# Kernel optimization log

Hardware: AMD Instinct MI355X
Metric: run time of the kernel (lower is better)

The kernel has to match this reference:

```python
import jax, jax.numpy as jnp
import numpy as np

TEMPERATURE = 0.07
CONCEPT_WEIGHT = 0.5
CONCEPT_SIM_WEIGHT = 0.3


def setup_inputs() -> dict:
    key = jax.random.key(0)
    k1, k2, k3, k4, k5 = jax.random.split(key, 5)
    B, C = 512, 256
    return {
        "logits_per_image": jax.random.normal(k1, (B, B), dtype=jnp.float32) * 3.0,
        "logits_per_text": jax.random.normal(k2, (B, B), dtype=jnp.float32) * 3.0,
        "concepts_logits": jax.random.normal(k3, (B, C), dtype=jnp.float32),
        "concepts_image_similarity": jax.random.normal(k4, (B, B), dtype=jnp.float32),
        # medical concepts in {-1 (missing), 0, 1}
        "medical_concepts": jax.random.randint(k5, (B, C), -1, 2, dtype=jnp.int32),
    }


def _clip_loss(logits_per_image, logits_per_text):
    # cross_entropy with labels = arange(B): -mean(diag(log_softmax))
    lp_img = jax.nn.log_softmax(logits_per_image, axis=1)
    lp_txt = jax.nn.log_softmax(logits_per_text, axis=1)
    image_loss = -jnp.mean(jnp.diagonal(lp_img))
    text_loss = -jnp.mean(jnp.diagonal(lp_txt))
    return (image_loss + text_loss) / 2.0


def _concept_classification_loss(concepts_logits, medical_concepts):
    mask = (medical_concepts != -1).astype(jnp.float32)
    targets = jnp.where(medical_concepts == -1, 0, medical_concepts).astype(jnp.float32)
    # BCEWithLogits (no pos_weight): logaddexp(0, x) - x*t  (numerically stable)
    loss = jnp.logaddexp(0.0, concepts_logits) - concepts_logits * targets
    return (loss * mask).sum() / (mask.sum() + 1e-8)


def _concept_similarity_loss(concepts_image_sim, medical_concepts):
    B = medical_concepts.shape[0]
    w = jnp.where(medical_concepts == -1, 0, medical_concepts).astype(jnp.float32)  # [B,C]
    # vectorized pairwise Jaccard (replaces O(B^2) python loop)
    intersection = jnp.minimum(w[:, None, :], w[None, :, :]).sum(-1)  # [B,B]
    union = jnp.maximum(w[:, None, :], w[None, :, :]).sum(-1)  # [B,B]
    sim = jnp.where(union > 0, intersection / jnp.where(union > 0, union, 1.0), 0.0)
    targets = jax.nn.softmax(sim / TEMPERATURE, axis=1)  # [B,B]
    log_probs = jax.nn.log_softmax(concepts_image_sim, axis=1)
    # kl_div(log_probs, targets, reduction='batchmean')
    kl = jnp.sum(targets * (jnp.log(targets) - log_probs)) / B
    return kl


def reference(logits_per_image, logits_per_text, concepts_logits,
              concepts_image_similarity, medical_concepts):
    clip_loss = _clip_loss(logits_per_image, logits_per_text)
    concept_loss = _concept_classification_loss(concepts_logits, medical_concepts)
    concept_sim_loss = _concept_similarity_loss(concepts_image_similarity, medical_concepts)
    total_loss = clip_loss + CONCEPT_WEIGHT * concept_loss + CONCEPT_SIM_WEIGHT * concept_sim_loss
    return total_loss
```

## Files before the change

kernel.cpp:

```cpp
#include <hip/hip_runtime.h>
#include <cstdint>

#define BSZ 512
#define CSZ 256


__device__ __forceinline__ float wave_sum64(float v) {
    #pragma unroll
    for (int o = 32; o > 0; o >>= 1) v += __shfl_xor(v, o, 64);
    return v;
}

__device__ __forceinline__ float block_sum(float v, float* s4) {
    v = wave_sum64(v);
    if ((threadIdx.x & 63) == 0) s4[threadIdx.x >> 6] = v;
    __syncthreads();
    float r = (s4[0] + s4[1]) + (s4[2] + s4[3]);
    __syncthreads();
    return r;
}

__global__ void __launch_bounds__(256)
prep(const float* __restrict__ img, const float* __restrict__ txt,
     const float* __restrict__ clog, const int* __restrict__ mc,
     char* __restrict__ ws) {
    __shared__ float s4[4];
    int g = blockIdx.x, tid = threadIdx.x;
    float* pc = (float*)(ws + 1024);
    float* pb = (float*)(ws + 5120);
    float* pm = (float*)(ws + 7168);
    unsigned long long* packed = (unsigned long long*)(ws + 12288);

    if (g == 0) ((unsigned int*)ws)[tid] = 0u;

    if (g < 1024) {
        int b = g & 511;
        const float* row = ((g < 512) ? img : txt) + (size_t)b * BSZ;
        float2 v = ((const float2*)row)[tid];
        float S = block_sum(expf(v.x) + expf(v.y), s4);
        if (tid == 0) pc[g] = logf(S) - row[b];
    } else {
        int b = g - 1024;
        int m = mc[b * CSZ + tid];
        float x = clog[b * CSZ + tid];
        float maskf = (m != -1) ? 1.0f : 0.0f;
        float t = (m == 1) ? 1.0f : 0.0f;
        float loss = (fmaxf(x, 0.0f) + log1pf(expf(-fabsf(x))) - x * t) * maskf;
        float Ls = block_sum(loss, s4);
        float Ms = block_sum(maskf, s4);
        if (tid == 0) { pb[b] = Ls; pm[b] = Ms; }
        unsigned long long bal = __ballot(m == 1);
        if ((tid & 63) == 0) packed[b * 4 + (tid >> 6)] = bal;
    }
}

__global__ void __launch_bounds__(256)
simfin(const float* __restrict__ csim, char* __restrict__ ws,
       float* __restrict__ out) {
    __shared__ float s4[4];
    __shared__ int islast;

    unsigned int* dc = (unsigned int*)ws;
    unsigned int* d2 = (unsigned int*)(ws + 512);
    float* pc = (float*)(ws + 1024);
    float* pb = (float*)(ws + 5120);
    float* pm = (float*)(ws + 7168);
    float* pk = (float*)(ws + 9216);
    const unsigned long long* packed = (const unsigned long long*)(ws + 12288);

    int b = blockIdx.x, tid = threadIdx.x;

    unsigned long long a0 = packed[b * 4 + 0], a1 = packed[b * 4 + 1];
    unsigned long long a2 = packed[b * 4 + 2], a3 = packed[b * 4 + 3];
    const ulonglong2* p2 = (const ulonglong2*)packed;
    ulonglong2 r0 = p2[4 * tid + 0], r1 = p2[4 * tid + 1];
    ulonglong2 r2 = p2[4 * tid + 2], r3 = p2[4 * tid + 3];
    float2 cv = ((const float2*)(csim + (size_t)b * BSZ))[tid];

    int i0 = __popcll(a0 & r0.x) + __popcll(a1 & r0.y) + __popcll(a2 & r1.x) + __popcll(a3 & r1.y);
    int u0 = __popcll(a0 | r0.x) + __popcll(a1 | r0.y) + __popcll(a2 | r1.x) + __popcll(a3 | r1.y);
    int i1 = __popcll(a0 & r2.x) + __popcll(a1 & r2.y) + __popcll(a2 & r3.x) + __popcll(a3 & r3.y);
    int u1 = __popcll(a0 | r2.x) + __popcll(a1 | r2.y) + __popcll(a2 | r3.x) + __popcll(a3 | r3.y);
    float s0 = ((u0 > 0) ? ((float)i0 / (float)u0) : 0.0f) * (1.0f / 0.07f);
    float s1 = ((u1 > 0) ? ((float)i1 / (float)u1) : 0.0f) * (1.0f / 0.07f);
    float c0 = cv.x, c1 = cv.y;

    float Zs = block_sum(expf(s0) + expf(s1), s4);
    float Zc = block_sum(expf(c0) + expf(c1), s4);
    float lse_s = logf(Zs), lse_c = logf(Zc);
    float t0 = expf(s0 - lse_s), t1 = expf(s1 - lse_s);
    float kl = block_sum(t0 * ((s0 - lse_s) - (c0 - lse_c)) +
                         t1 * ((s1 - lse_s) - (c1 - lse_c)), s4);

    if (tid == 0) {
        __hip_atomic_store(&pk[b], kl, __ATOMIC_RELAXED, __HIP_MEMORY_SCOPE_AGENT);
        __threadfence();
        islast = 0;
        unsigned t1k = atomicAdd(&dc[(b & 7) * 16], 1u);
        if (t1k == 63u) {
            unsigned t2k = atomicAdd(d2, 1u);
            if (t2k == 7u) islast = 1;
        }
    }
    __syncthreads();

    if (islast) {
        __threadfence();
        float sc = 0.0f, sb = 0.0f, sm = 0.0f, sk = 0.0f;
        for (int k = tid; k < 2 * BSZ; k += 256) sc += pc[k];
        for (int k = tid; k < BSZ; k += 256) {
            sb += pb[k];
            sm += pm[k];
            sk += __hip_atomic_load(&pk[k], __ATOMIC_RELAXED, __HIP_MEMORY_SCOPE_AGENT);
        }
        sc = block_sum(sc, s4);
        sb = block_sum(sb, s4);
        sm = block_sum(sm, s4);
        sk = block_sum(sk, s4);
        if (tid == 0) {
            out[0] = sc / (2.0f * BSZ)
                   + 0.5f * (sb / (sm + 1e-8f))
                   + 0.3f * (sk / (float)BSZ);
        }
    }
}

extern "C" void kernel_launch(void* const* d_in, const int* in_sizes, int n_in,
                              void* d_out, int out_size, void* d_ws, size_t ws_size,
                              hipStream_t stream) {
    const float* logits_img = (const float*)d_in[0];
    const float* logits_txt = (const float*)d_in[1];
    const float* clog       = (const float*)d_in[2];
    const float* csim       = (const float*)d_in[3];
    const int*   mc         = (const int*)d_in[4];
    float* out = (float*)d_out;
    char* ws = (char*)d_ws;

    prep<<<3 * BSZ, 256, 0, stream>>>(logits_img, logits_txt, clog, mc, ws);
    simfin<<<BSZ, 256, 0, stream>>>(csim, ws, out);
}
```

Before: 79.34 us.

## Fuse prep and similarity kernels into one cooperative kernel with grid syncs

Merges the two launches into a single cooperative kernel of 512 blocks. Each block handles one row of every input in phase one, then a grid.sync stands in for the kernel boundary before the Jaccard/KL phase, and a second grid.sync replaces the atomic-counter last-block detection for the final reduction. It also batches several block reductions into one shared-memory pass. The aim is to remove a launch gap and the counter atomics, at the cost of two grid-wide barriers, the overhead of a cooperative launch, and a smaller grid in phase one.

```diff
diff --git a/kernel.cpp b/kernel.cpp
--- a/kernel.cpp
+++ b/kernel.cpp
@@ -1,126 +1,144 @@
 #include <hip/hip_runtime.h>
+#include <hip/hip_cooperative_groups.h>
 #include <cstdint>
+
+namespace cg = cooperative_groups;
 
 #define BSZ 512
 #define CSZ 256
 
 
 __device__ __forceinline__ float wave_sum64(float v) {
-    #pragma unroll
+#pragma unroll
     for (int o = 32; o > 0; o >>= 1) v += __shfl_xor(v, o, 64);
     return v;
 }
 
-__device__ __forceinline__ float block_sum(float v, float* s4) {
-    v = wave_sum64(v);
-    if ((threadIdx.x & 63) == 0) s4[threadIdx.x >> 6] = v;
-    __syncthreads();
-    float r = (s4[0] + s4[1]) + (s4[2] + s4[3]);
-    __syncthreads();
-    return r;
+__device__ __forceinline__ void ast(float* p, float v) {
+    __hip_atomic_store(p, v, __ATOMIC_RELAXED, __HIP_MEMORY_SCOPE_AGENT);
+}
+__device__ __forceinline__ float ald(const float* p) {
+    return __hip_atomic_load(p, __ATOMIC_RELAXED, __HIP_MEMORY_SCOPE_AGENT);
+}
+__device__ __forceinline__ void astu(unsigned long long* p, unsigned long long v) {
+    __hip_atomic_store(p, v, __ATOMIC_RELAXED, __HIP_MEMORY_SCOPE_AGENT);
+}
+__device__ __forceinline__ unsigned long long aldu(const unsigned long long* p) {
+    return __hip_atomic_load(p, __ATOMIC_RELAXED, __HIP_MEMORY_SCOPE_AGENT);
 }
 
 __global__ void __launch_bounds__(256)
-prep(const float* __restrict__ img, const float* __restrict__ txt,
-     const float* __restrict__ clog, const int* __restrict__ mc,
-     char* __restrict__ ws) {
-    __shared__ float s4[4];
-    int g = blockIdx.x, tid = threadIdx.x;
-    float* pc = (float*)(ws + 1024);
-    float* pb = (float*)(ws + 5120);
-    float* pm = (float*)(ws + 7168);
-    unsigned long long* packed = (unsigned long long*)(ws + 12288);
-
-    if (g == 0) ((unsigned int*)ws)[tid] = 0u;
-
-    if (g < 1024) {
-        int b = g & 511;
-        const float* row = ((g < 512) ? img : txt) + (size_t)b * BSZ;
-        float2 v = ((const float2*)row)[tid];
-        float S = block_sum(expf(v.x) + expf(v.y), s4);
-        if (tid == 0) pc[g] = logf(S) - row[b];
-    } else {
-        int b = g - 1024;
-        int m = mc[b * CSZ + tid];
-        float x = clog[b * CSZ + tid];
-        float maskf = (m != -1) ? 1.0f : 0.0f;
-        float t = (m == 1) ? 1.0f : 0.0f;
-        float loss = (fmaxf(x, 0.0f) + log1pf(expf(-fabsf(x))) - x * t) * maskf;
-        float Ls = block_sum(loss, s4);
-        float Ms = block_sum(maskf, s4);
-        if (tid == 0) { pb[b] = Ls; pm[b] = Ms; }
-        unsigned long long bal = __ballot(m == 1);
-        if ((tid & 63) == 0) packed[b * 4 + (tid >> 6)] = bal;
-    }
-}
-
-__global__ void __launch_bounds__(256)
-simfin(const float* __restrict__ csim, char* __restrict__ ws,
-       float* __restrict__ out) {
-    __shared__ float s4[4];
-    __shared__ int islast;
-
-    unsigned int* dc = (unsigned int*)ws;
-    unsigned int* d2 = (unsigned int*)(ws + 512);
-    float* pc = (float*)(ws + 1024);
-    float* pb = (float*)(ws + 5120);
-    float* pm = (float*)(ws + 7168);
-    float* pk = (float*)(ws + 9216);
-    const unsigned long long* packed = (const unsigned long long*)(ws + 12288);
+fused(const float* __restrict__ img, const float* __restrict__ txt,
+      const float* __restrict__ clog, const float* __restrict__ csim,
+      const int* __restrict__ mc, char* __restrict__ ws,
+      float* __restrict__ out) {
+    __shared__ float red[4][4];
+    cg::grid_group grid = cg::this_grid();
 
     int b = blockIdx.x, tid = threadIdx.x;
+    int w = tid >> 6, lane = tid & 63;
 
-    unsigned long long a0 = packed[b * 4 + 0], a1 = packed[b * 4 + 1];
-    unsigned long long a2 = packed[b * 4 + 2], a3 = packed[b * 4 + 3];
-    const ulonglong2* p2 = (const ulonglong2*)packed;
-    ulonglong2 r0 = p2[4 * tid + 0], r1 = p2[4 * tid + 1];
-    ulonglong2 r2 = p2[4 * tid + 2], r3 = p2[4 * tid + 3];
+    float* pc = (float*)(ws);
+    float* pb = (float*)(ws + 4096);
+    float* pm = (float*)(ws + 6144);
+    float* pk = (float*)(ws + 8192);
+    unsigned long long* packed = (unsigned long long*)(ws + 10240);
+
+    const float* irow = img + (size_t)b * BSZ;
+    const float* trow = txt + (size_t)b * BSZ;
+    float2 iv = ((const float2*)irow)[tid];
+    float2 tv = ((const float2*)trow)[tid];
+    int   m = mc[b * CSZ + tid];
+    float x = clog[b * CSZ + tid];
     float2 cv = ((const float2*)(csim + (size_t)b * BSZ))[tid];
 
-    int i0 = __popcll(a0 & r0.x) + __popcll(a1 & r0.y) + __popcll(a2 & r1.x) + __popcll(a3 & r1.y);
-    int u0 = __popcll(a0 | r0.x) + __popcll(a1 | r0.y) + __popcll(a2 | r1.x) + __popcll(a3 | r1.y);
-    int i1 = __popcll(a0 & r2.x) + __popcll(a1 & r2.y) + __popcll(a2 & r3.x) + __popcll(a3 & r3.y);
-    int u1 = __popcll(a0 | r2.x) + __popcll(a1 | r2.y) + __popcll(a2 | r3.x) + __popcll(a3 | r3.y);
+    float maskf = (m != -1) ? 1.0f : 0.0f;
+    float tgt   = (m == 1) ? 1.0f : 0.0f;
+    float bce = (fmaxf(x, 0.0f) + log1pf(expf(-fabsf(x))) - x * tgt) * maskf;
+
+    float vI = wave_sum64(expf(iv.x) + expf(iv.y));
+    float vT = wave_sum64(expf(tv.x) + expf(tv.y));
+    float vB = wave_sum64(bce);
+    float vM = wave_sum64(maskf);
+    if (lane == 0) {
+        red[w][0] = vI; red[w][1] = vT; red[w][2] = vB; red[w][3] = vM;
+    }
+    unsigned long long bal = __ballot(m == 1);
+    if (lane == 0) astu(&packed[b * 4 + w], bal);
+    __syncthreads();
+    if (tid == 0) {
+        float Si = (red[0][0] + red[1][0]) + (red[2][0] + red[3][0]);
+        float St = (red[0][1] + red[1][1]) + (red[2][1] + red[3][1]);
+        float Sb = (red[0][2] + red[1][2]) + (red[2][2] + red[3][2]);
+        float Sm = (red[0][3] + red[1][3]) + (red[2][3] + red[3][3]);
+        ast(&pc[b],       logf(Si) - irow[b]);
+        ast(&pc[BSZ + b], logf(St) - trow[b]);
+        ast(&pb[b], Sb);
+        ast(&pm[b], Sm);
+    }
+
+    grid.sync();
+
+    unsigned long long a0 = aldu(&packed[b * 4 + 0]);
+    unsigned long long a1 = aldu(&packed[b * 4 + 1]);
+    unsigned long long a2 = aldu(&packed[b * 4 + 2]);
+    unsigned long long a3 = aldu(&packed[b * 4 + 3]);
+    const unsigned long long* pr = packed + (size_t)tid * 8;
+    unsigned long long r0 = aldu(pr + 0), r1 = aldu(pr + 1);
+    unsigned long long r2 = aldu(pr + 2), r3 = aldu(pr + 3);
+    unsigned long long r4 = aldu(pr + 4), r5 = aldu(pr + 5);
+    unsigned long long r6 = aldu(pr + 6), r7 = aldu(pr + 7);
+
+    int i0 = __popcll(a0 & r0) + __popcll(a1 & r1) + __popcll(a2 & r2) + __popcll(a3 & r3);
+    int u0 = __popcll(a0 | r0) + __popcll(a1 | r1) + __popcll(a2 | r2) + __popcll(a3 | r3);
+    int i1 = __popcll(a0 & r4) + __popcll(a1 & r5) + __popcll(a2 & r6) + __popcll(a3 & r7);
+    int u1 = __popcll(a0 | r4) + __popcll(a1 | r5) + __popcll(a2 | r6) + __popcll(a3 | r7);
     float s0 = ((u0 > 0) ? ((float)i0 / (float)u0) : 0.0f) * (1.0f / 0.07f);
     float s1 = ((u1 > 0) ? ((float)i1 / (float)u1) : 0.0f) * (1.0f / 0.07f);
-    float c0 = cv.x, c1 = cv.y;
 
-    float Zs = block_sum(expf(s0) + expf(s1), s4);
-    float Zc = block_sum(expf(c0) + expf(c1), s4);
+    float zs = wave_sum64(expf(s0) + expf(s1));
+    float zc = wave_sum64(expf(cv.x) + expf(cv.y));
+    if (lane == 0) { red[w][0] = zs; red[w][1] = zc; }
+    __syncthreads();
+    float Zs = (red[0][0] + red[1][0]) + (red[2][0] + red[3][0]);
+    float Zc = (red[0][1] + red[1][1]) + (red[2][1] + red[3][1]);
     float lse_s = logf(Zs), lse_c = logf(Zc);
     float t0 = expf(s0 - lse_s), t1 = expf(s1 - lse_s);
-    float kl = block_sum(t0 * ((s0 - lse_s) - (c0 - lse_c)) +
-                         t1 * ((s1 - lse_s) - (c1 - lse_c)), s4);
+    float klv = wave_sum64(t0 * ((s0 - lse_s) - (cv.x - lse_c)) +
+                           t1 * ((s1 - lse_s) - (cv.y - lse_c)));
+    if (lane == 0) red[w][2] = klv;
+    __syncthreads();
+    if (tid == 0) {
+        float Sk = (red[0][2] + red[1][2]) + (red[2][2] + red[3][2]);
+        ast(&pk[b], Sk);
+    }
 
-    if (tid == 0) {
-        __hip_atomic_store(&pk[b], kl, __ATOMIC_RELAXED, __HIP_MEMORY_SCOPE_AGENT);
-        __threadfence();
-        islast = 0;
-        unsigned t1k = atomicAdd(&dc[(b & 7) * 16], 1u);
-        if (t1k == 63u) {
-            unsigned t2k = atomicAdd(d2, 1u);
-            if (t2k == 7u) islast = 1;
+    grid.sync();
+
+    if (b == 0) {
+        float sc = 0.0f, sb = 0.0f, sm = 0.0f, sk = 0.0f;
+        for (int k = tid; k < 2 * BSZ; k += 256) sc += ald(&pc[k]);
+        for (int k = tid; k < BSZ; k += 256) {
+            sb += ald(&pb[k]);
+            sm += ald(&pm[k]);
+            sk += ald(&pk[k]);
         }
-    }
-    __syncthreads();
-
-    if (islast) {
-        __threadfence();
-        float sc = 0.0f, sb = 0.0f, sm = 0.0f, sk = 0.0f;
-        for (int k = tid; k < 2 * BSZ; k += 256) sc += pc[k];
-        for (int k = tid; k < BSZ; k += 256) {
-            sb += pb[k];
-            sm += pm[k];
-            sk += __hip_atomic_load(&pk[k], __ATOMIC_RELAXED, __HIP_MEMORY_SCOPE_AGENT);
+        sc = wave_sum64(sc);
+        sb = wave_sum64(sb);
+        sm = wave_sum64(sm);
+        sk = wave_sum64(sk);
+        if (lane == 0) {
+            red[w][0] = sc; red[w][1] = sb; red[w][2] = sm; red[w][3] = sk;
         }
-        sc = block_sum(sc, s4);
-        sb = block_sum(sb, s4);
-        sm = block_sum(sm, s4);
-        sk = block_sum(sk, s4);
+        __syncthreads();
         if (tid == 0) {
-            out[0] = sc / (2.0f * BSZ)
-                   + 0.5f * (sb / (sm + 1e-8f))
-                   + 0.3f * (sk / (float)BSZ);
+            float Sc = (red[0][0] + red[1][0]) + (red[2][0] + red[3][0]);
+            float Sb = (red[0][1] + red[1][1]) + (red[2][1] + red[3][1]);
+            float Sm = (red[0][2] + red[1][2]) + (red[2][2] + red[3][2]);
+            float Sk = (red[0][3] + red[1][3]) + (red[2][3] + red[3][3]);
+            out[0] = Sc / (2.0f * BSZ)
+                   + 0.5f * (Sb / (Sm + 1e-8f))
+                   + 0.3f * (Sk / (float)BSZ);
         }
     }
 }
@@ -136,6 +154,8 @@
     float* out = (float*)d_out;
     char* ws = (char*)d_ws;
 
-    prep<<<3 * BSZ, 256, 0, stream>>>(logits_img, logits_txt, clog, mc, ws);
-    simfin<<<BSZ, 256, 0, stream>>>(csim, ws, out);
+    void* args[] = {(void*)&logits_img, (void*)&logits_txt, (void*)&clog,
+                    (void*)&csim, (void*)&mc, (void*)&ws, (void*)&out};
+    hipLaunchCooperativeKernel((void*)fused, dim3(BSZ), dim3(256),
+                               args, 0, stream);
 }
```

New measurement: 185.9 us. +134.3%, slower.

## Merge prep block roles into one block per row and batch block reductions

Applied to the files above, without the earlier changes.

The prep kernel previously ran three kinds of blocks (image rows, text rows, concept rows). It now runs one block per batch index that handles the image row, the text row and the concept row together. Multiple reductions are batched so each block shares one shared-memory exchange and a single __syncthreads, instead of two barriers per block_sum call. This cuts the grid size and barrier count and raises memory-level parallelism per block. The cost is fewer blocks to hide latency on a large GPU.

```diff
diff --git a/kernel.cpp b/kernel.cpp
--- a/kernel.cpp
+++ b/kernel.cpp
@@ -6,58 +6,65 @@
 
 
 __device__ __forceinline__ float wave_sum64(float v) {
-    #pragma unroll
+#pragma unroll
     for (int o = 32; o > 0; o >>= 1) v += __shfl_xor(v, o, 64);
     return v;
-}
-
-__device__ __forceinline__ float block_sum(float v, float* s4) {
-    v = wave_sum64(v);
-    if ((threadIdx.x & 63) == 0) s4[threadIdx.x >> 6] = v;
-    __syncthreads();
-    float r = (s4[0] + s4[1]) + (s4[2] + s4[3]);
-    __syncthreads();
-    return r;
 }
 
 __global__ void __launch_bounds__(256)
 prep(const float* __restrict__ img, const float* __restrict__ txt,
      const float* __restrict__ clog, const int* __restrict__ mc,
      char* __restrict__ ws) {
-    __shared__ float s4[4];
-    int g = blockIdx.x, tid = threadIdx.x;
+    __shared__ float red[4][4];
+    int b = blockIdx.x, tid = threadIdx.x;
+    int w = tid >> 6, lane = tid & 63;
+
     float* pc = (float*)(ws + 1024);
     float* pb = (float*)(ws + 5120);
     float* pm = (float*)(ws + 7168);
     unsigned long long* packed = (unsigned long long*)(ws + 12288);
 
-    if (g == 0) ((unsigned int*)ws)[tid] = 0u;
+    if (b == 0) ((unsigned int*)ws)[tid] = 0u;
 
-    if (g < 1024) {
-        int b = g & 511;
-        const float* row = ((g < 512) ? img : txt) + (size_t)b * BSZ;
-        float2 v = ((const float2*)row)[tid];
-        float S = block_sum(expf(v.x) + expf(v.y), s4);
-        if (tid == 0) pc[g] = logf(S) - row[b];
-    } else {
-        int b = g - 1024;
-        int m = mc[b * CSZ + tid];
-        float x = clog[b * CSZ + tid];
-        float maskf = (m != -1) ? 1.0f : 0.0f;
-        float t = (m == 1) ? 1.0f : 0.0f;
-        float loss = (fmaxf(x, 0.0f) + log1pf(expf(-fabsf(x))) - x * t) * maskf;
-        float Ls = block_sum(loss, s4);
-        float Ms = block_sum(maskf, s4);
-        if (tid == 0) { pb[b] = Ls; pm[b] = Ms; }
-        unsigned long long bal = __ballot(m == 1);
-        if ((tid & 63) == 0) packed[b * 4 + (tid >> 6)] = bal;
+    const float* irow = img + (size_t)b * BSZ;
+    const float* trow = txt + (size_t)b * BSZ;
+    float2 iv = ((const float2*)irow)[tid];
+    float2 tv = ((const float2*)trow)[tid];
+    int   m = mc[b * CSZ + tid];
+    float x = clog[b * CSZ + tid];
+    float di = irow[b];
+    float dt = trow[b];
+
+    float maskf = (m != -1) ? 1.0f : 0.0f;
+    float tgt   = (m == 1) ? 1.0f : 0.0f;
+    float bce = (fmaxf(x, 0.0f) + log1pf(expf(-fabsf(x))) - x * tgt) * maskf;
+
+    float vI = wave_sum64(expf(iv.x) + expf(iv.y));
+    float vT = wave_sum64(expf(tv.x) + expf(tv.y));
+    float vB = wave_sum64(bce);
+    float vM = wave_sum64(maskf);
+    if (lane == 0) {
+        red[w][0] = vI; red[w][1] = vT; red[w][2] = vB; red[w][3] = vM;
+    }
+    unsigned long long bal = __ballot(m == 1);
+    if (lane == 0) packed[b * 4 + w] = bal;
+    __syncthreads();
+    if (tid == 0) {
+        float Si = (red[0][0] + red[1][0]) + (red[2][0] + red[3][0]);
+        float St = (red[0][1] + red[1][1]) + (red[2][1] + red[3][1]);
+        float Sb = (red[0][2] + red[1][2]) + (red[2][2] + red[3][2]);
+        float Sm = (red[0][3] + red[1][3]) + (red[2][3] + red[3][3]);
+        pc[b]       = logf(Si) - di;
+        pc[BSZ + b] = logf(St) - dt;
+        pb[b] = Sb;
+        pm[b] = Sm;
     }
 }
 
 __global__ void __launch_bounds__(256)
 simfin(const float* __restrict__ csim, char* __restrict__ ws,
        float* __restrict__ out) {
-    __shared__ float s4[4];
+    __shared__ float red[4][4];
     __shared__ int islast;
 
     unsigned int* dc = (unsigned int*)ws;
@@ -69,13 +76,14 @@
     const unsigned long long* packed = (const unsigned long long*)(ws + 12288);
 
     int b = blockIdx.x, tid = threadIdx.x;
+    int w = tid >> 6, lane = tid & 63;
 
+    float2 cv = ((const float2*)(csim + (size_t)b * BSZ))[tid];
     unsigned long long a0 = packed[b * 4 + 0], a1 = packed[b * 4 + 1];
     unsigned long long a2 = packed[b * 4 + 2], a3 = packed[b * 4 + 3];
     const ulonglong2* p2 = (const ulonglong2*)packed;
     ulonglong2 r0 = p2[4 * tid + 0], r1 = p2[4 * tid + 1];
     ulonglong2 r2 = p2[4 * tid + 2], r3 = p2[4 * tid + 3];
-    float2 cv = ((const float2*)(csim + (size_t)b * BSZ))[tid];
 
     int i0 = __popcll(a0 & r0.x) + __popcll(a1 & r0.y) + __popcll(a2 & r1.x) + __popcll(a3 & r1.y);
     int u0 = __popcll(a0 | r0.x) + __popcll(a1 | r0.y) + __popcll(a2 | r1.x) + __popcll(a3 | r1.y);
@@ -85,14 +93,21 @@
     float s1 = ((u1 > 0) ? ((float)i1 / (float)u1) : 0.0f) * (1.0f / 0.07f);
     float c0 = cv.x, c1 = cv.y;
 
-    float Zs = block_sum(expf(s0) + expf(s1), s4);
-    float Zc = block_sum(expf(c0) + expf(c1), s4);
+    float zs = wave_sum64(expf(s0) + expf(s1));
+    float zc = wave_sum64(expf(c0) + expf(c1));
+    if (lane == 0) { red[w][0] = zs; red[w][1] = zc; }
+    __syncthreads();
+    float Zs = (red[0][0] + red[1][0]) + (red[2][0] + red[3][0]);
+    float Zc = (red[0][1] + red[1][1]) + (red[2][1] + red[3][1]);
     float lse_s = logf(Zs), lse_c = logf(Zc);
     float t0 = expf(s0 - lse_s), t1 = expf(s1 - lse_s);
-    float kl = block_sum(t0 * ((s0 - lse_s) - (c0 - lse_c)) +
-                         t1 * ((s1 - lse_s) - (c1 - lse_c)), s4);
+    float klv = wave_sum64(t0 * ((s0 - lse_s) - (c0 - lse_c)) +
+                           t1 * ((s1 - lse_s) - (c1 - lse_c)));
+    if (lane == 0) red[w][2] = klv;
+    __syncthreads();
 
     if (tid == 0) {
+        float kl = (red[0][2] + red[1][2]) + (red[2][2] + red[3][2]);
         __hip_atomic_store(&pk[b], kl, __ATOMIC_RELAXED, __HIP_MEMORY_SCOPE_AGENT);
         __threadfence();
         islast = 0;
@@ -113,14 +128,22 @@
             sm += pm[k];
             sk += __hip_atomic_load(&pk[k], __ATOMIC_RELAXED, __HIP_MEMORY_SCOPE_AGENT);
         }
-        sc = block_sum(sc, s4);
-        sb = block_sum(sb, s4);
-        sm = block_sum(sm, s4);
-        sk = block_sum(sk, s4);
+        sc = wave_sum64(sc);
+        sb = wave_sum64(sb);
+        sm = wave_sum64(sm);
+        sk = wave_sum64(sk);
+        if (lane == 0) {
+            red[w][0] = sc; red[w][1] = sb; red[w][2] = sm; red[w][3] = sk;
+        }
+        __syncthreads();
         if (tid == 0) {
-            out[0] = sc / (2.0f * BSZ)
-                   + 0.5f * (sb / (sm + 1e-8f))
-                   + 0.3f * (sk / (float)BSZ);
+            float Sc = (red[0][0] + red[1][0]) + (red[2][0] + red[3][0]);
+            float Sb = (red[0][1] + red[1][1]) + (red[2][1] + red[3][1]);
+            float Sm = (red[0][2] + red[1][2]) + (red[2][2] + red[3][2]);
+            float Sk = (red[0][3] + red[1][3]) + (red[2][3] + red[3][3]);
+            out[0] = Sc / (2.0f * BSZ)
+                   + 0.5f * (Sb / (Sm + 1e-8f))
+                   + 0.3f * (Sk / (float)BSZ);
         }
     }
 }
@@ -136,6 +159,6 @@
     float* out = (float*)d_out;
     char* ws = (char*)d_ws;
 
-    prep<<<3 * BSZ, 256, 0, stream>>>(logits_img, logits_txt, clog, mc, ws);
+    prep<<<BSZ, 256, 0, stream>>>(logits_img, logits_txt, clog, mc, ws);
     simfin<<<BSZ, 256, 0, stream>>>(csim, ws, out);
 }
```

Result: faster. 77.43 us (-2.4%).
